# Optimization experiments

Hardware: AMD Instinct MI355X
Metric: run time of the kernel (lower is better)

The kernel has to match this reference:

```python
import jax, jax.numpy as jnp
import numpy as np

N_NODES = 100000
D_FEAT = 128
K_NEIGH = 16
N_LAYERS = 2
F_OUT = 128  # features = [128, 128]


def setup_inputs() -> dict:
    key = jax.random.key(0)
    k1, k2, k3 = jax.random.split(key, 3)
    feats = jax.random.normal(k1, (N_NODES, D_FEAT), dtype=jnp.float32)
    # per-layer sampled neighbor indices (fresh sampling each layer, as in the source)
    neigh_idx = jax.random.randint(k2, (N_LAYERS, N_NODES, K_NEIGH), 0, N_NODES, dtype=jnp.int32)
    # Dense kernels: input is concat(self, mean_neighbors) -> 2*D; both layers 256 -> 128
    Ws = jax.random.normal(k3, (N_LAYERS, 2 * D_FEAT, F_OUT), dtype=jnp.float32) * (1.0 / np.sqrt(2 * D_FEAT))
    bs = jnp.zeros((N_LAYERS, F_OUT), dtype=jnp.float32)
    return {"feats": feats, "neigh_idx": neigh_idx, "Ws": Ws, "bs": bs}


def reference(feats, neigh_idx, Ws, bs):
    """GraphSAGE (mean aggregator): per layer, gather sampled neighbors,
    mean-aggregate, concat with self, Dense; relu between layers.
    Returns the last-layer Dense output (pre-relu), matching `new_feats`
    returned by the source module.
    """
    h = feats  # [N, D]
    z = h
    for l in range(Ws.shape[0]):
        neigh = h[neigh_idx[l]]              # [N, K, D] irregular gather
        agg = neigh.mean(axis=1)             # [N, D] mean aggregation
        cat = jnp.concatenate([h, agg], axis=-1)  # [N, 2D]
        z = cat @ Ws[l] + bs[l]              # [N, F]
        h = jax.nn.relu(z)
    return z
```

## Files before the change

kernel.cpp:

```cpp
#include <hip/hip_runtime.h>

#define N_NODES 100000
#define D 128
#define K 16
#define CATK 256
#define MB 32
#define PAD 8
#define LDSW (CATK + PAD)
#define ZW 132

typedef __attribute__((ext_vector_type(8))) short bf16x8;
typedef __attribute__((ext_vector_type(4))) float f32x4;
typedef __attribute__((ext_vector_type(2))) float f32x2;

__device__ __forceinline__ unsigned short f2bf(float f) {
    union { float f; unsigned u; } v; v.f = f;
    unsigned u = v.u;
    return (unsigned short)((u + 0x7fffu + ((u >> 16) & 1u)) >> 16);
}

__device__ __forceinline__ unsigned pk4(float a, float b, float c, float d) {
    int w = __builtin_amdgcn_cvt_pk_fp8_f32(a, b, 0, false);
    w = __builtin_amdgcn_cvt_pk_fp8_f32(c, d, w, true);
    return (unsigned)w;
}

__device__ __forceinline__ void dec4p(unsigned w, f32x2* a) {
    f32x2 lo = __builtin_amdgcn_cvt_pk_f32_fp8((int)w, false);
    f32x2 hi = __builtin_amdgcn_cvt_pk_f32_fp8((int)w, true);
    a[0] += lo;
    a[1] += hi;
}

__global__ void cvt_all(const float* __restrict__ feats, const float* __restrict__ Ws,
                        unsigned* __restrict__ f8, unsigned short* __restrict__ Wt) {
    int tid = blockIdx.x * 256 + threadIdx.x;
    int i = tid * 16;
    if (i < N_NODES * D) {
        const float4* p = (const float4*)(feats + i);
        float4 v0 = p[0], v1 = p[1], v2 = p[2], v3 = p[3];
        uint4 o;
        o.x = pk4(v0.x, v0.y, v0.z, v0.w);
        o.y = pk4(v1.x, v1.y, v1.z, v1.w);
        o.z = pk4(v2.x, v2.y, v2.z, v2.w);
        o.w = pk4(v3.x, v3.y, v3.z, v3.w);
        *(uint4*)(f8 + i / 4) = o;
    }
    if (tid < 2 * CATK * D) {
        int l = tid / (CATK * D);
        int r = tid % (CATK * D);
        int n = r / CATK, k = r % CATK;
        Wt[tid] = f2bf(Ws[l * CATK * D + k * D + n]);
    }
}

template <int LAYER>
__launch_bounds__(256, 6)
__global__ void sage_layer(const float* __restrict__ self_f32,
                           const unsigned short* __restrict__ self_bf,
                           const unsigned char* __restrict__ g8,
                           const int* __restrict__ idx,
                           const unsigned short* __restrict__ Wt,
                           const float* __restrict__ bias,
                           unsigned short* __restrict__ h_out,
                           unsigned char* __restrict__ h8_out,
                           float* __restrict__ z_out) {
    __shared__ __align__(16) char smraw[MB * LDSW * 2];
    unsigned short (*cat)[LDSW] = (unsigned short (*)[LDSW])smraw;
    float (*zb)[ZW] = (float (*)[ZW])smraw;

    const int t = threadIdx.x;
    const int base = blockIdx.x * MB;
    const int lane = t & 63;
    const int wave = t >> 6;
    const int q = lane >> 4;
    const int nlo = lane & 15;

    {
        const int m = t >> 3;
        const int c = (t & 7) * 16;
        const int node = base + m;

        const int4* ip = (const int4*)(idx + (size_t)node * K);
        int4 i0 = ip[0], i1 = ip[1];

        if (LAYER == 0) {
            const float4* sp = (const float4*)(self_f32 + (size_t)node * D + c);
            float sv[16];
            *(f32x4*)&sv[0]  = *(const f32x4*)&sp[0];
            *(f32x4*)&sv[4]  = *(const f32x4*)&sp[1];
            *(f32x4*)&sv[8]  = *(const f32x4*)&sp[2];
            *(f32x4*)&sv[12] = *(const f32x4*)&sp[3];
            unsigned w[8];
#pragma unroll
            for (int j = 0; j < 8; ++j)
                w[j] = (unsigned)f2bf(sv[2 * j]) | ((unsigned)f2bf(sv[2 * j + 1]) << 16);
            *(uint4*)&cat[m][c]     = make_uint4(w[0], w[1], w[2], w[3]);
            *(uint4*)&cat[m][c + 8] = make_uint4(w[4], w[5], w[6], w[7]);
        } else {
            const uint4* sp = (const uint4*)(self_bf + (size_t)node * D + c);
            uint4 sb0 = sp[0], sb1 = sp[1];
            *(uint4*)&cat[m][c]     = sb0;
            *(uint4*)&cat[m][c + 8] = sb1;
        }

        const unsigned char* gp = g8 + c;
        f32x2 acc2[8];
#pragma unroll
        for (int j = 0; j < 8; ++j) acc2[j] = (f32x2){0.f, 0.f};

        {
            uint4 u[8];
            u[0] = *(const uint4*)(gp + (size_t)i0.x * D);
            u[1] = *(const uint4*)(gp + (size_t)i0.y * D);
            u[2] = *(const uint4*)(gp + (size_t)i0.z * D);
            u[3] = *(const uint4*)(gp + (size_t)i0.w * D);
            u[4] = *(const uint4*)(gp + (size_t)i1.x * D);
            u[5] = *(const uint4*)(gp + (size_t)i1.y * D);
            u[6] = *(const uint4*)(gp + (size_t)i1.z * D);
            u[7] = *(const uint4*)(gp + (size_t)i1.w * D);
            int4 i2 = ip[2], i3 = ip[3];
#pragma unroll
            for (int k = 0; k < 8; ++k) {
                dec4p(u[k].x, acc2 + 0);
                dec4p(u[k].y, acc2 + 2);
                dec4p(u[k].z, acc2 + 4);
                dec4p(u[k].w, acc2 + 6);
            }
            u[0] = *(const uint4*)(gp + (size_t)i2.x * D);
            u[1] = *(const uint4*)(gp + (size_t)i2.y * D);
            u[2] = *(const uint4*)(gp + (size_t)i2.z * D);
            u[3] = *(const uint4*)(gp + (size_t)i2.w * D);
            u[4] = *(const uint4*)(gp + (size_t)i3.x * D);
            u[5] = *(const uint4*)(gp + (size_t)i3.y * D);
            u[6] = *(const uint4*)(gp + (size_t)i3.z * D);
            u[7] = *(const uint4*)(gp + (size_t)i3.w * D);
#pragma unroll
            for (int k = 0; k < 8; ++k) {
                dec4p(u[k].x, acc2 + 0);
                dec4p(u[k].y, acc2 + 2);
                dec4p(u[k].z, acc2 + 4);
                dec4p(u[k].w, acc2 + 6);
            }
        }

        unsigned pk[8];
#pragma unroll
        for (int j = 0; j < 8; ++j) {
            unsigned short a = f2bf(acc2[j].x * (1.f / 16.f));
            unsigned short b = f2bf(acc2[j].y * (1.f / 16.f));
            pk[j] = (unsigned)a | ((unsigned)b << 16);
        }
        *(uint4*)&cat[m][D + c]     = make_uint4(pk[0], pk[1], pk[2], pk[3]);
        *(uint4*)&cat[m][D + c + 8] = make_uint4(pk[4], pk[5], pk[6], pk[7]);
    }

    bf16x8 bfrag[2][8];
#pragma unroll
    for (int ct = 0; ct < 2; ++ct) {
        int n = wave * 32 + ct * 16 + nlo;
        const unsigned short* wp = Wt + n * CATK + q * 8;
#pragma unroll
        for (int ks = 0; ks < 8; ++ks)
            bfrag[ct][ks] = *(const bf16x8*)(wp + ks * 32);
    }

    __syncthreads();

    f32x4 acc00 = {}, acc01 = {}, acc10 = {}, acc11 = {};
#pragma unroll
    for (int ks = 0; ks < 8; ++ks) {
        bf16x8 a0 = *(const bf16x8*)&cat[nlo][ks * 32 + q * 8];
        bf16x8 a1 = *(const bf16x8*)&cat[16 + nlo][ks * 32 + q * 8];
        acc00 = __builtin_amdgcn_mfma_f32_16x16x32_bf16(a0, bfrag[0][ks], acc00, 0, 0, 0);
        acc01 = __builtin_amdgcn_mfma_f32_16x16x32_bf16(a0, bfrag[1][ks], acc01, 0, 0, 0);
        acc10 = __builtin_amdgcn_mfma_f32_16x16x32_bf16(a1, bfrag[0][ks], acc10, 0, 0, 0);
        acc11 = __builtin_amdgcn_mfma_f32_16x16x32_bf16(a1, bfrag[1][ks], acc11, 0, 0, 0);
    }

    if (LAYER == 1) {
#pragma unroll
        for (int ct = 0; ct < 2; ++ct) {
            int col = wave * 32 + ct * 16 + nlo;
            float bv = bias[col];
            f32x4 v0 = (ct == 0) ? acc00 : acc01;
            f32x4 v1 = (ct == 0) ? acc10 : acc11;
#pragma unroll
            for (int r = 0; r < 4; ++r) {
                z_out[(size_t)(base + q * 4 + r) * D + col]      = v0[r] + bv;
                z_out[(size_t)(base + 16 + q * 4 + r) * D + col] = v1[r] + bv;
            }
        }
        return;
    }

    __syncthreads();
#pragma unroll
    for (int ct = 0; ct < 2; ++ct) {
        int col = wave * 32 + ct * 16 + nlo;
        float bv = bias[col];
        f32x4 v0 = (ct == 0) ? acc00 : acc01;
        f32x4 v1 = (ct == 0) ? acc10 : acc11;
#pragma unroll
        for (int r = 0; r < 4; ++r) {
            zb[q * 4 + r][col]      = v0[r] + bv;
            zb[16 + q * 4 + r][col] = v1[r] + bv;
        }
    }
    __syncthreads();
    {
        const int m = t >> 3;
        const int c = (t & 7) * 16;
        float x[16];
        *(f32x4*)&x[0]  = *(const f32x4*)&zb[m][c];
        *(f32x4*)&x[4]  = *(const f32x4*)&zb[m][c + 4];
        *(f32x4*)&x[8]  = *(const f32x4*)&zb[m][c + 8];
        *(f32x4*)&x[12] = *(const f32x4*)&zb[m][c + 12];
        size_t go = (size_t)(base + m) * D + c;
#pragma unroll
        for (int i = 0; i < 16; ++i) x[i] = x[i] > 0.f ? x[i] : 0.f;
        unsigned wb[8];
#pragma unroll
        for (int j = 0; j < 8; ++j)
            wb[j] = (unsigned)f2bf(x[2 * j]) | ((unsigned)f2bf(x[2 * j + 1]) << 16);
        uint4* hp = (uint4*)(h_out + go);
        hp[0] = make_uint4(wb[0], wb[1], wb[2], wb[3]);
        hp[1] = make_uint4(wb[4], wb[5], wb[6], wb[7]);
        uint4 o8;
        o8.x = pk4(x[0], x[1], x[2], x[3]);
        o8.y = pk4(x[4], x[5], x[6], x[7]);
        o8.z = pk4(x[8], x[9], x[10], x[11]);
        o8.w = pk4(x[12], x[13], x[14], x[15]);
        *(uint4*)(h8_out + go) = o8;
    }
}

extern "C" void kernel_launch(void* const* d_in, const int* in_sizes, int n_in,
                              void* d_out, int out_size, void* d_ws, size_t ws_size,
                              hipStream_t stream) {
    const float* feats = (const float*)d_in[0];
    const int* neigh   = (const int*)d_in[1];
    const float* Ws    = (const float*)d_in[2];
    const float* bs    = (const float*)d_in[3];
    float* out = (float*)d_out;

    char* ws = (char*)d_ws;
    unsigned short* h1_bf  = (unsigned short*)(ws);
    unsigned char*  feats8 = (unsigned char*)(ws + 25600000);
    unsigned char*  h18    = (unsigned char*)(ws + 38400000);
    unsigned short* Wt     = (unsigned short*)(ws + 51200000);

    cvt_all<<<3125, 256, 0, stream>>>(feats, Ws, (unsigned*)feats8, Wt);

    sage_layer<0><<<N_NODES / MB, 256, 0, stream>>>(
        feats, nullptr, feats8, neigh, Wt, bs, h1_bf, h18, nullptr);
    sage_layer<1><<<N_NODES / MB, 256, 0, stream>>>(
        nullptr, h1_bf, h18, neigh + N_NODES * K, Wt + CATK * D, bs + D,
        nullptr, nullptr, out);
}
```

Baseline: 219.5 us.

## Shrink node tile to 16 rows with 128-thread blocks and inline weight loads

Halves the per-block node tile from 32 to 16 rows and the block from 256 to 128 threads, so each wave now computes 64 output columns over a single 16-row A fragment. The weight fragments are no longer preloaded into registers; they are loaded from global memory inside the MFMA loop. This lowers LDS use and register pressure and doubles the number of blocks. The cost is that weight loads per node double, since each weight tile is now reused across only 16 rows. The gather section and the hidden unseen code must also fit the new thread mapping, which is not visible.

```diff
diff --git a/kernel.cpp b/kernel.cpp
--- a/kernel.cpp
+++ b/kernel.cpp
@@ -4,7 +4,8 @@
 #define D 128
 #define K 16
 #define CATK 256
-#define MB 32
+#define MB 16
+#define NT 128
 #define PAD 8
 #define LDSW (CATK + PAD)
 #define ZW 132
@@ -55,7 +56,7 @@
 }
 
 template <int LAYER>
-__launch_bounds__(256, 6)
+__launch_bounds__(NT, 4)
 __global__ void sage_layer(const float* __restrict__ self_f32,
                            const unsigned short* __restrict__ self_bf,
                            const unsigned char* __restrict__ g8,
@@ -155,57 +156,40 @@
         *(uint4*)&cat[m][D + c + 8] = make_uint4(pk[4], pk[5], pk[6], pk[7]);
     }
 
-    bf16x8 bfrag[2][8];
-#pragma unroll
-    for (int ct = 0; ct < 2; ++ct) {
-        int n = wave * 32 + ct * 16 + nlo;
-        const unsigned short* wp = Wt + n * CATK + q * 8;
-#pragma unroll
-        for (int ks = 0; ks < 8; ++ks)
-            bfrag[ct][ks] = *(const bf16x8*)(wp + ks * 32);
-    }
-
     __syncthreads();
 
-    f32x4 acc00 = {}, acc01 = {}, acc10 = {}, acc11 = {};
+    f32x4 acc[4] = {{}, {}, {}, {}};
 #pragma unroll
     for (int ks = 0; ks < 8; ++ks) {
         bf16x8 a0 = *(const bf16x8*)&cat[nlo][ks * 32 + q * 8];
-        bf16x8 a1 = *(const bf16x8*)&cat[16 + nlo][ks * 32 + q * 8];
-        acc00 = __builtin_amdgcn_mfma_f32_16x16x32_bf16(a0, bfrag[0][ks], acc00, 0, 0, 0);
-        acc01 = __builtin_amdgcn_mfma_f32_16x16x32_bf16(a0, bfrag[1][ks], acc01, 0, 0, 0);
-        acc10 = __builtin_amdgcn_mfma_f32_16x16x32_bf16(a1, bfrag[0][ks], acc10, 0, 0, 0);
-        acc11 = __builtin_amdgcn_mfma_f32_16x16x32_bf16(a1, bfrag[1][ks], acc11, 0, 0, 0);
+#pragma unroll
+        for (int ct = 0; ct < 4; ++ct) {
+            int n = wave * 64 + ct * 16 + nlo;
+            bf16x8 b = *(const bf16x8*)(Wt + n * CATK + ks * 32 + q * 8);
+            acc[ct] = __builtin_amdgcn_mfma_f32_16x16x32_bf16(a0, b, acc[ct], 0, 0, 0);
+        }
     }
 
     if (LAYER == 1) {
 #pragma unroll
-        for (int ct = 0; ct < 2; ++ct) {
-            int col = wave * 32 + ct * 16 + nlo;
+        for (int ct = 0; ct < 4; ++ct) {
+            int col = wave * 64 + ct * 16 + nlo;
             float bv = bias[col];
-            f32x4 v0 = (ct == 0) ? acc00 : acc01;
-            f32x4 v1 = (ct == 0) ? acc10 : acc11;
-#pragma unroll
-            for (int r = 0; r < 4; ++r) {
-                z_out[(size_t)(base + q * 4 + r) * D + col]      = v0[r] + bv;
-                z_out[(size_t)(base + 16 + q * 4 + r) * D + col] = v1[r] + bv;
-            }
+#pragma unroll
+            for (int r = 0; r < 4; ++r)
+                z_out[(size_t)(base + q * 4 + r) * D + col] = acc[ct][r] + bv;
         }
         return;
     }
 
     __syncthreads();
 #pragma unroll
-    for (int ct = 0; ct < 2; ++ct) {
-        int col = wave * 32 + ct * 16 + nlo;
+    for (int ct = 0; ct < 4; ++ct) {
+        int col = wave * 64 + ct * 16 + nlo;
         float bv = bias[col];
-        f32x4 v0 = (ct == 0) ? acc00 : acc01;
-        f32x4 v1 = (ct == 0) ? acc10 : acc11;
-#pragma unroll
-        for (int r = 0; r < 4; ++r) {
-            zb[q * 4 + r][col]      = v0[r] + bv;
-            zb[16 + q * 4 + r][col] = v1[r] + bv;
-        }
+#pragma unroll
+        for (int r = 0; r < 4; ++r)
+            zb[q * 4 + r][col] = acc[ct][r] + bv;
     }
     __syncthreads();
     {
@@ -252,9 +236,9 @@
 
     cvt_all<<<3125, 256, 0, stream>>>(feats, Ws, (unsigned*)feats8, Wt);
 
-    sage_layer<0><<<N_NODES / MB, 256, 0, stream>>>(
+    sage_layer<0><<<N_NODES / MB, NT, 0, stream>>>(
         feats, nullptr, feats8, neigh, Wt, bs, h1_bf, h18, nullptr);
-    sage_layer<1><<<N_NODES / MB, 256, 0, stream>>>(
+    sage_layer<1><<<N_NODES / MB, NT, 0, stream>>>(
         nullptr, h1_bf, h18, neigh + N_NODES * K, Wt + CATK * D, bs + D,
         nullptr, nullptr, out);
 }
```

Result: slower. 245.3 us (+11.8%).

## Split fused gather-mean and matmul into separate kernels per layer

Applied to the files above, without the earlier changes.

Moves the fp8 neighbor gather and mean aggregation into a standalone kernel that writes a bf16 aggregate buffer, and makes the layer kernel read that buffer instead of gathering. The aim is to decouple the latency-bound irregular gather from the MFMA matmul so that each can run at its own occupancy. This costs an extra global write and read of the aggregate per layer, plus two additional kernel launches.

```diff
diff --git a/kernel.cpp b/kernel.cpp
--- a/kernel.cpp
+++ b/kernel.cpp
@@ -54,17 +54,80 @@
     }
 }
 
+__launch_bounds__(256, 4)
+__global__ void gather_mean(const unsigned char* __restrict__ g8,
+                            const int* __restrict__ idx,
+                            unsigned short* __restrict__ agg) {
+    const int t = threadIdx.x;
+    const int m = t >> 3;
+    const int c = (t & 7) * 16;
+    const int node = blockIdx.x * MB + m;
+
+    const int4* ip = (const int4*)(idx + (size_t)node * K);
+    int4 i0 = ip[0], i1 = ip[1];
+
+    const unsigned char* gp = g8 + c;
+    f32x2 acc2[8];
+#pragma unroll
+    for (int j = 0; j < 8; ++j) acc2[j] = (f32x2){0.f, 0.f};
+
+    {
+        uint4 u[8];
+        u[0] = *(const uint4*)(gp + (size_t)i0.x * D);
+        u[1] = *(const uint4*)(gp + (size_t)i0.y * D);
+        u[2] = *(const uint4*)(gp + (size_t)i0.z * D);
+        u[3] = *(const uint4*)(gp + (size_t)i0.w * D);
+        u[4] = *(const uint4*)(gp + (size_t)i1.x * D);
+        u[5] = *(const uint4*)(gp + (size_t)i1.y * D);
+        u[6] = *(const uint4*)(gp + (size_t)i1.z * D);
+        u[7] = *(const uint4*)(gp + (size_t)i1.w * D);
+        int4 i2 = ip[2], i3 = ip[3];
+#pragma unroll
+        for (int k = 0; k < 8; ++k) {
+            dec4p(u[k].x, acc2 + 0);
+            dec4p(u[k].y, acc2 + 2);
+            dec4p(u[k].z, acc2 + 4);
+            dec4p(u[k].w, acc2 + 6);
+        }
+        u[0] = *(const uint4*)(gp + (size_t)i2.x * D);
+        u[1] = *(const uint4*)(gp + (size_t)i2.y * D);
+        u[2] = *(const uint4*)(gp + (size_t)i2.z * D);
+        u[3] = *(const uint4*)(gp + (size_t)i2.w * D);
+        u[4] = *(const uint4*)(gp + (size_t)i3.x * D);
+        u[5] = *(const uint4*)(gp + (size_t)i3.y * D);
+        u[6] = *(const uint4*)(gp + (size_t)i3.z * D);
+        u[7] = *(const uint4*)(gp + (size_t)i3.w * D);
+#pragma unroll
+        for (int k = 0; k < 8; ++k) {
+            dec4p(u[k].x, acc2 + 0);
+            dec4p(u[k].y, acc2 + 2);
+            dec4p(u[k].z, acc2 + 4);
+            dec4p(u[k].w, acc2 + 6);
+        }
+    }
+
+    unsigned pk[8];
+#pragma unroll
+    for (int j = 0; j < 8; ++j) {
+        unsigned short a = f2bf(acc2[j].x * (1.f / 16.f));
+        unsigned short b = f2bf(acc2[j].y * (1.f / 16.f));
+        pk[j] = (unsigned)a | ((unsigned)b << 16);
+    }
+    unsigned short* op = agg + (size_t)node * D + c;
+    *(uint4*)op       = make_uint4(pk[0], pk[1], pk[2], pk[3]);
+    *(uint4*)(op + 8) = make_uint4(pk[4], pk[5], pk[6], pk[7]);
+}
+
 template <int LAYER>
-__launch_bounds__(256, 6)
-__global__ void sage_layer(const float* __restrict__ self_f32,
-                           const unsigned short* __restrict__ self_bf,
-                           const unsigned char* __restrict__ g8,
-                           const int* __restrict__ idx,
-                           const unsigned short* __restrict__ Wt,
-                           const float* __restrict__ bias,
-                           unsigned short* __restrict__ h_out,
-                           unsigned char* __restrict__ h8_out,
-                           float* __restrict__ z_out) {
+__launch_bounds__(256, 4)
+__global__ void sage_mm(const float* __restrict__ self_f32,
+                        const unsigned short* __restrict__ self_bf,
+                        const unsigned short* __restrict__ agg,
+                        const unsigned short* __restrict__ Wt,
+                        const float* __restrict__ bias,
+                        unsigned short* __restrict__ h_out,
+                        unsigned char* __restrict__ h8_out,
+                        float* __restrict__ z_out) {
     __shared__ __align__(16) char smraw[MB * LDSW * 2];
     unsigned short (*cat)[LDSW] = (unsigned short (*)[LDSW])smraw;
     float (*zb)[ZW] = (float (*)[ZW])smraw;
@@ -81,8 +144,8 @@
         const int c = (t & 7) * 16;
         const int node = base + m;
 
-        const int4* ip = (const int4*)(idx + (size_t)node * K);
-        int4 i0 = ip[0], i1 = ip[1];
+        const uint4* ap = (const uint4*)(agg + (size_t)node * D + c);
+        uint4 a0 = ap[0], a1 = ap[1];
 
         if (LAYER == 0) {
             const float4* sp = (const float4*)(self_f32 + (size_t)node * D + c);
@@ -104,55 +167,8 @@
             *(uint4*)&cat[m][c + 8] = sb1;
         }
 
-        const unsigned char* gp = g8 + c;
-        f32x2 acc2[8];
-#pragma unroll
-        for (int j = 0; j < 8; ++j) acc2[j] = (f32x2){0.f, 0.f};
-
-        {
-            uint4 u[8];
-            u[0] = *(const uint4*)(gp + (size_t)i0.x * D);
-            u[1] = *(const uint4*)(gp + (size_t)i0.y * D);
-            u[2] = *(const uint4*)(gp + (size_t)i0.z * D);
-            u[3] = *(const uint4*)(gp + (size_t)i0.w * D);
-            u[4] = *(const uint4*)(gp + (size_t)i1.x * D);
-            u[5] = *(const uint4*)(gp + (size_t)i1.y * D);
-            u[6] = *(const uint4*)(gp + (size_t)i1.z * D);
-            u[7] = *(const uint4*)(gp + (size_t)i1.w * D);
-            int4 i2 = ip[2], i3 = ip[3];
-#pragma unroll
-            for (int k = 0; k < 8; ++k) {
-                dec4p(u[k].x, acc2 + 0);
-                dec4p(u[k].y, acc2 + 2);
-                dec4p(u[k].z, acc2 + 4);
-                dec4p(u[k].w, acc2 + 6);
-            }
-            u[0] = *(const uint4*)(gp + (size_t)i2.x * D);
-            u[1] = *(const uint4*)(gp + (size_t)i2.y * D);
-            u[2] = *(const uint4*)(gp + (size_t)i2.z * D);
-            u[3] = *(const uint4*)(gp + (size_t)i2.w * D);
-            u[4] = *(const uint4*)(gp + (size_t)i3.x * D);
-            u[5] = *(const uint4*)(gp + (size_t)i3.y * D);
-            u[6] = *(const uint4*)(gp + (size_t)i3.z * D);
-            u[7] = *(const uint4*)(gp + (size_t)i3.w * D);
-#pragma unroll
-            for (int k = 0; k < 8; ++k) {
-                dec4p(u[k].x, acc2 + 0);
-                dec4p(u[k].y, acc2 + 2);
-                dec4p(u[k].z, acc2 + 4);
-                dec4p(u[k].w, acc2 + 6);
-            }
-        }
-
-        unsigned pk[8];
-#pragma unroll
-        for (int j = 0; j < 8; ++j) {
-            unsigned short a = f2bf(acc2[j].x * (1.f / 16.f));
-            unsigned short b = f2bf(acc2[j].y * (1.f / 16.f));
-            pk[j] = (unsigned)a | ((unsigned)b << 16);
-        }
-        *(uint4*)&cat[m][D + c]     = make_uint4(pk[0], pk[1], pk[2], pk[3]);
-        *(uint4*)&cat[m][D + c + 8] = make_uint4(pk[4], pk[5], pk[6], pk[7]);
+        *(uint4*)&cat[m][D + c]     = a0;
+        *(uint4*)&cat[m][D + c + 8] = a1;
     }
 
     bf16x8 bfrag[2][8];
@@ -249,12 +265,16 @@
     unsigned char*  feats8 = (unsigned char*)(ws + 25600000);
     unsigned char*  h18    = (unsigned char*)(ws + 38400000);
     unsigned short* Wt     = (unsigned short*)(ws + 51200000);
+    unsigned short* agg    = (unsigned short*)(ws + 51331072);
 
     cvt_all<<<3125, 256, 0, stream>>>(feats, Ws, (unsigned*)feats8, Wt);
 
-    sage_layer<0><<<N_NODES / MB, 256, 0, stream>>>(
-        feats, nullptr, feats8, neigh, Wt, bs, h1_bf, h18, nullptr);
-    sage_layer<1><<<N_NODES / MB, 256, 0, stream>>>(
-        nullptr, h1_bf, h18, neigh + N_NODES * K, Wt + CATK * D, bs + D,
+    gather_mean<<<N_NODES / MB, 256, 0, stream>>>(feats8, neigh, agg);
+    sage_mm<0><<<N_NODES / MB, 256, 0, stream>>>(
+        feats, nullptr, agg, Wt, bs, h1_bf, h18, nullptr);
+
+    gather_mean<<<N_NODES / MB, 256, 0, stream>>>(h18, neigh + N_NODES * K, agg);
+    sage_mm<1><<<N_NODES / MB, 256, 0, stream>>>(
+        nullptr, h1_bf, agg, Wt + CATK * D, bs + D,
         nullptr, nullptr, out);
 }
```

New measurement: 219.7 us. About the same (+0.1%).
